# Optimization experiments

Hardware: AMD Instinct MI355X
Metric: run time of the kernel (lower is better)

## Reference

```python
import jax, jax.numpy as jnp
import numpy as np

N_ATOM, N_BOND, N_MOL, D = 250000, 250000, 10000, 64
BN_EPS = 1e-5


def _bn(x, gamma, beta):
    # torch BatchNorm1d training-mode math (biased variance)
    m = jnp.mean(x, axis=0)
    v = jnp.var(x, axis=0)
    return (x - m) * jax.lax.rsqrt(v + BN_EPS) * gamma + beta


def setup_inputs() -> dict:
    key = jax.random.key(0)
    ks = jax.random.split(key, 12)
    h = jax.random.normal(ks[0], (N_ATOM, D), jnp.float32)
    e = jax.random.normal(ks[1], (N_BOND, D), jnp.float32)
    u = jax.random.normal(ks[2], (N_MOL, D), jnp.float32)
    norm_atom = jax.random.uniform(ks[3], (N_ATOM, 1), jnp.float32)
    norm_bond = jax.random.uniform(ks[4], (N_BOND, 1), jnp.float32)
    bond_u = jax.random.randint(ks[5], (N_BOND,), 0, N_ATOM, jnp.int32)
    bond_v = jax.random.randint(ks[6], (N_BOND,), 0, N_ATOM, jnp.int32)
    atom2mol = jax.random.randint(ks[7], (N_ATOM,), 0, N_MOL, jnp.int32)
    bond2mol = jax.random.randint(ks[8], (N_BOND,), 0, N_MOL, jnp.int32)
    # 9 Linear layers A..I stacked: order A,B,C,D,E,F,G,H,I
    Ws = jax.random.normal(ks[9], (9, D, D), jnp.float32) * 0.05
    bs = jax.random.normal(ks[10], (9, D), jnp.float32) * 0.05
    bn_gamma = jnp.ones((3, D), jnp.float32)   # [e, h, u]
    bn_beta = jnp.zeros((3, D), jnp.float32)
    return dict(h=h, e=e, u=u, norm_atom=norm_atom, norm_bond=norm_bond,
                Ws=Ws, bs=bs, bn_gamma=bn_gamma, bn_beta=bn_beta,
                bond_u=bond_u, bond_v=bond_v, atom2mol=atom2mol, bond2mol=bond2mol)


def reference(h, e, u, norm_atom, norm_bond, Ws, bs, bn_gamma, bn_beta,
              bond_u, bond_v, atom2mol, bond2mol):
    lin = lambda x, i: x @ Ws[i] + bs[i]
    Ah, Dh, Eh = lin(h, 0), lin(h, 3), lin(h, 4)
    Be = lin(e, 1)
    Cu, Fu = lin(u, 2), lin(u, 5)

    # bond update: a2b (sum of Ah of both endpoints) + b2b self-loop + g2b broadcast
    e_new = Ah[bond_u] + Ah[bond_v] + Be + Cu[bond2mol]
    e_new = e_new * norm_bond                  # graph_norm
    e_new = _bn(e_new, bn_gamma[0], bn_beta[0])
    e_new = jax.nn.elu(e_new)

    # atom update: a2a self-loop + gated b2a (select_not_equal == other endpoint's Eh) + g2a
    sig = jax.nn.sigmoid(e_new)                # [N_BOND, D]
    dst = jnp.concatenate([bond_u, bond_v])    # each bond sends to both endpoints
    Eh_other = jnp.concatenate([Eh[bond_v], Eh[bond_u]])
    sig2 = jnp.concatenate([sig, sig])
    num = jax.ops.segment_sum(sig2 * Eh_other, dst, num_segments=N_ATOM)
    den = jax.ops.segment_sum(sig2, dst, num_segments=N_ATOM) + 1e-6
    h_new = Dh + num / den + Fu[atom2mol]
    h_new = h_new * norm_atom                  # graph_norm
    h_new = _bn(h_new, bn_gamma[1], bn_beta[1])
    h_new = jax.nn.elu(h_new)

    # global update: mean(Gh over atoms) + mean(He over bonds) + g2g self-loop Iu
    Gh, He, Iu = lin(h_new, 6), lin(e_new, 7), lin(u, 8)
    cnt_a = jax.ops.segment_sum(jnp.ones((N_ATOM, 1), h.dtype), atom2mol, num_segments=N_MOL)
    cnt_b = jax.ops.segment_sum(jnp.ones((N_BOND, 1), e.dtype), bond2mol, num_segments=N_MOL)
    u_new = (jax.ops.segment_sum(Gh, atom2mol, num_segments=N_MOL) / jnp.maximum(cnt_a, 1.0)
             + jax.ops.segment_sum(He, bond2mol, num_segments=N_MOL) / jnp.maximum(cnt_b, 1.0)
             + Iu)
    u_new = _bn(u_new, bn_gamma[2], bn_beta[2])
    u_new = jax.nn.elu(u_new)

    return h_new, e_new, u_new
```

## Files before the change

kernel.cpp:

```cpp
#include <hip/hip_runtime.h>
#include <cmath>

#define DD 64
#define TILE 64
#define BLK 256
#define NSLOT 64

__device__ __forceinline__ float elu_f(float x) {
  return x > 0.f ? x : expm1f(x);
}
__device__ __forceinline__ float sigmoid_fast(float x) {
  return __builtin_amdgcn_rcpf(1.f + __expf(-x));
}

__device__ __forceinline__ void fma4(float4& a, float s, const float4 b) {
  a.x = fmaf(s, b.x, a.x);
  a.y = fmaf(s, b.y, a.y);
  a.z = fmaf(s, b.z, a.z);
  a.w = fmaf(s, b.w, a.w);
}
__device__ __forceinline__ void add4(float4& a, const float4 b) {
  a.x += b.x; a.y += b.y; a.z += b.z; a.w += b.w;
}
__device__ __forceinline__ void sqacc4(float4& a, const float4 b) {
  a.x = fmaf(b.x, b.x, a.x);
  a.y = fmaf(b.y, b.y, a.y);
  a.z = fmaf(b.z, b.z, a.z);
  a.w = fmaf(b.w, b.w, a.w);
}
__device__ __forceinline__ void scale4(float4& a, float s) {
  a.x *= s; a.y *= s; a.z *= s; a.w *= s;
}

__device__ __forceinline__ void matmul_tile(const float (*xs)[DD + 4], const float (*wl)[DD],
                                            int r0, int c0, float4 acc[4]) {
#pragma unroll 2
  for (int k0 = 0; k0 < DD; k0 += 4) {
    float4 x0 = *(const float4*)&xs[r0 + 0][k0];
    float4 x1 = *(const float4*)&xs[r0 + 1][k0];
    float4 x2 = *(const float4*)&xs[r0 + 2][k0];
    float4 x3 = *(const float4*)&xs[r0 + 3][k0];
    float4 w0 = *(const float4*)&wl[k0 + 0][c0];
    float4 w1 = *(const float4*)&wl[k0 + 1][c0];
    float4 w2 = *(const float4*)&wl[k0 + 2][c0];
    float4 w3 = *(const float4*)&wl[k0 + 3][c0];
    fma4(acc[0], x0.x, w0); fma4(acc[0], x0.y, w1); fma4(acc[0], x0.z, w2); fma4(acc[0], x0.w, w3);
    fma4(acc[1], x1.x, w0); fma4(acc[1], x1.y, w1); fma4(acc[1], x1.z, w2); fma4(acc[1], x1.w, w3);
    fma4(acc[2], x2.x, w0); fma4(acc[2], x2.y, w1); fma4(acc[2], x2.z, w2); fma4(acc[2], x2.w, w3);
    fma4(acc[3], x3.x, w0); fma4(acc[3], x3.y, w1); fma4(acc[3], x3.z, w2); fma4(acc[3], x3.w, w3);
  }
}

__global__ void cnt_kernel(const int* __restrict__ a2m, int na,
                           const int* __restrict__ b2m, int nb,
                           const int* __restrict__ bu, const int* __restrict__ bv,
                           int* __restrict__ cnta_i, int* __restrict__ cntb_i,
                           int* __restrict__ deg) {
  int i = blockIdx.x * blockDim.x + threadIdx.x;
  if (i < na) {
    atomicAdd(&cnta_i[a2m[i]], 1);
  } else if (i < na + nb) {
    int b = i - na;
    atomicAdd(&cntb_i[b2m[b]], 1);
    atomicAdd(&deg[bu[b]], 1);
    atomicAdd(&deg[bv[b]], 1);
  }
}

__global__ void seg_alloc_kernel(const int* __restrict__ deg, int n,
                                 int* __restrict__ start, int* __restrict__ gcount) {
  int i = blockIdx.x * blockDim.x + threadIdx.x;
  int lane = threadIdx.x & 63;
  int d = (i < n) ? deg[i] : 0;
  int pre = d;
#pragma unroll
  for (int off = 1; off < 64; off <<= 1) {
    int t = __shfl_up(pre, off, 64);
    if (lane >= off) pre += t;
  }
  int total = __shfl(pre, 63, 64);
  int excl = pre - d;
  int base = 0;
  if (lane == 63) base = atomicAdd(gcount, total);
  base = __shfl(base, 63, 64);
  if (i < n) start[i] = base + excl;
}

__global__ void fill_kernel(const int* __restrict__ bu, const int* __restrict__ bv, int nb,
                            const int* __restrict__ start, int* __restrict__ cur,
                            int2* __restrict__ adj) {
  int b = blockIdx.x * blockDim.x + threadIdx.x;
  if (b < nb) {
    int a0 = bu[b], a1 = bv[b];
    int p = start[a0] + atomicAdd(&cur[a0], 1);
    adj[p] = make_int2(b, a1);
    int q = start[a1] + atomicAdd(&cur[a1], 1);
    adj[q] = make_int2(b, a0);
  }
}

__global__ void fill_mol_kernel(const int* __restrict__ a2m, int na,
                                const int* __restrict__ b2m, int nb,
                                const int* __restrict__ start_ma, int* __restrict__ cur_ma,
                                int* __restrict__ lista,
                                const int* __restrict__ start_mb, int* __restrict__ cur_mb,
                                int* __restrict__ listb) {
  int i = blockIdx.x * blockDim.x + threadIdx.x;
  if (i < na) {
    int m = a2m[i];
    lista[start_ma[m] + atomicAdd(&cur_ma[m], 1)] = i;
  } else if (i < na + nb) {
    int b = i - na;
    int m = b2m[b];
    listb[start_mb[m] + atomicAdd(&cur_mb[m], 1)] = b;
  }
}

__global__ __launch_bounds__(BLK) void lin2_kernel(
    const float* __restrict__ x, int nrows,
    const float* __restrict__ W0, const float* __restrict__ b0, float* __restrict__ out0,
    const float* __restrict__ W1, const float* __restrict__ b1, float* __restrict__ out1) {
  __shared__ __align__(16) float xs[TILE][DD + 4];
  __shared__ __align__(16) float w0[DD][DD];
  __shared__ __align__(16) float w1[DD][DD];
  const int tid = threadIdx.x;
  const int base = blockIdx.x * TILE;
  int rows = nrows - base; if (rows > TILE) rows = TILE;
  for (int l = tid; l < DD * DD; l += BLK) {
    int r = l >> 6, c = l & 63;
    xs[r][c] = (r < rows) ? x[(size_t)(base + r) * DD + c] : 0.f;
    w0[r][c] = W0[l];
    w1[r][c] = W1[l];
  }
  __syncthreads();
  const int tr = tid >> 4, tc = tid & 15;
  const int r0 = tr * 4, c0 = tc * 4;
  float4 accA[4], accB[4];
#pragma unroll
  for (int i = 0; i < 4; ++i) {
    accA[i] = make_float4(0.f, 0.f, 0.f, 0.f);
    accB[i] = make_float4(0.f, 0.f, 0.f, 0.f);
  }
#pragma unroll 1
  for (int k0 = 0; k0 < DD; k0 += 4) {
    float4 x0 = *(const float4*)&xs[r0 + 0][k0];
    float4 x1 = *(const float4*)&xs[r0 + 1][k0];
    float4 x2 = *(const float4*)&xs[r0 + 2][k0];
    float4 x3 = *(const float4*)&xs[r0 + 3][k0];
    float4 wa0 = *(const float4*)&w0[k0 + 0][c0];
    float4 wa1 = *(const float4*)&w0[k0 + 1][c0];
    float4 wa2 = *(const float4*)&w0[k0 + 2][c0];
    float4 wa3 = *(const float4*)&w0[k0 + 3][c0];
    float4 wb0 = *(const float4*)&w1[k0 + 0][c0];
    float4 wb1 = *(const float4*)&w1[k0 + 1][c0];
    float4 wb2 = *(const float4*)&w1[k0 + 2][c0];
    float4 wb3 = *(const float4*)&w1[k0 + 3][c0];
    fma4(accA[0], x0.x, wa0); fma4(accA[0], x0.y, wa1); fma4(accA[0], x0.z, wa2); fma4(accA[0], x0.w, wa3);
    fma4(accA[1], x1.x, wa0); fma4(accA[1], x1.y, wa1); fma4(accA[1], x1.z, wa2); fma4(accA[1], x1.w, wa3);
    fma4(accA[2], x2.x, wa0); fma4(accA[2], x2.y, wa1); fma4(accA[2], x2.z, wa2); fma4(accA[2], x2.w, wa3);
    fma4(accA[3], x3.x, wa0); fma4(accA[3], x3.y, wa1); fma4(accA[3], x3.z, wa2); fma4(accA[3], x3.w, wa3);
    fma4(accB[0], x0.x, wb0); fma4(accB[0], x0.y, wb1); fma4(accB[0], x0.z, wb2); fma4(accB[0], x0.w, wb3);
    fma4(accB[1], x1.x, wb0); fma4(accB[1], x1.y, wb1); fma4(accB[1], x1.z, wb2); fma4(accB[1], x1.w, wb3);
    fma4(accB[2], x2.x, wb0); fma4(accB[2], x2.y, wb1); fma4(accB[2], x2.z, wb2); fma4(accB[2], x2.w, wb3);
    fma4(accB[3], x3.x, wb0); fma4(accB[3], x3.y, wb1); fma4(accB[3], x3.z, wb2); fma4(accB[3], x3.w, wb3);
  }
  float4 bv0 = *(const float4*)&b0[c0];
  float4 bv1 = *(const float4*)&b1[c0];
#pragma unroll
  for (int i = 0; i < 4; ++i) {
    if (r0 + i < rows) {
      size_t rb = (size_t)(base + r0 + i) * DD + c0;
      float4 o0 = accA[i]; add4(o0, bv0);
      float4 o1 = accB[i]; add4(o1, bv1);
      *(float4*)&out0[rb] = o0;
      *(float4*)&out1[rb] = o1;
    }
  }
}

__global__ __launch_bounds__(BLK) void lin1_kernel(
    const float* __restrict__ x, int nrows,
    const float* __restrict__ W, const float* __restrict__ b, float* __restrict__ out) {
  __shared__ __align__(16) float xs[TILE][DD + 4];
  __shared__ __align__(16) float wl[DD][DD];
  const int tid = threadIdx.x;
  const int base = blockIdx.x * TILE;
  int rows = nrows - base; if (rows > TILE) rows = TILE;
  for (int l = tid; l < DD * DD; l += BLK) {
    int r = l >> 6, c = l & 63;
    xs[r][c] = (r < rows) ? x[(size_t)(base + r) * DD + c] : 0.f;
    wl[r][c] = W[l];
  }
  __syncthreads();
  const int tr = tid >> 4, tc = tid & 15;
  const int r0 = tr * 4, c0 = tc * 4;
  float4 acc[4];
#pragma unroll
  for (int i = 0; i < 4; ++i) acc[i] = make_float4(0.f, 0.f, 0.f, 0.f);
  matmul_tile(xs, wl, r0, c0, acc);
  float4 bv = *(const float4*)&b[c0];
#pragma unroll
  for (int i = 0; i < 4; ++i) {
    if (r0 + i < rows) {
      size_t rb = (size_t)(base + r0 + i) * DD + c0;
      float4 o = acc[i]; add4(o, bv);
      *(float4*)&out[rb] = o;
    }
  }
}

__global__ __launch_bounds__(BLK) void bond1_kernel(
    const float* __restrict__ e, int nrows, int ntiles,
    const float* __restrict__ W1, const float* __restrict__ b1,
    const float* __restrict__ Ah, const float* __restrict__ Cu,
    const int* __restrict__ bu, const int* __restrict__ bv, const int* __restrict__ b2m,
    const float* __restrict__ nrm,
    float* __restrict__ e_pre,
    float* __restrict__ ssum, float* __restrict__ ssq) {
  __shared__ __align__(16) float xs[TILE][DD + 4];
  __shared__ __align__(16) float wl[DD][DD];
  __shared__ int sbu[TILE], sbv[TILE], sbm[TILE];
  __shared__ float snb[TILE];
  __shared__ __align__(16) float red[16][DD];
  const int tid = threadIdx.x;
  const int tr = tid >> 4, tc = tid & 15, r0 = tr * 4, c0 = tc * 4;
  for (int l = tid; l < DD * DD; l += BLK) wl[l >> 6][l & 63] = W1[l];
  float4 bp = *(const float4*)&b1[c0];
  float4 lsum = make_float4(0.f, 0.f, 0.f, 0.f);
  float4 lsq  = make_float4(0.f, 0.f, 0.f, 0.f);
  for (int tile = blockIdx.x; tile < ntiles; tile += gridDim.x) {
    const int base = tile * TILE;
    int rows = nrows - base; if (rows > TILE) rows = TILE;
    __syncthreads();
    for (int l = tid; l < TILE * DD; l += BLK) {
      int r = l >> 6, c = l & 63;
      xs[r][c] = (r < rows) ? e[(size_t)(base + r) * DD + c] : 0.f;
    }
    if (tid < TILE) {
      bool v = tid < rows;
      int rb = base + tid;
      sbu[tid] = v ? bu[rb] : 0;
      sbv[tid] = v ? bv[rb] : 0;
      sbm[tid] = v ? b2m[rb] : 0;
      snb[tid] = v ? nrm[rb] : 0.f;
    }
    __syncthreads();
    float4 acc[4];
#pragma unroll
    for (int i = 0; i < 4; ++i) acc[i] = make_float4(0.f, 0.f, 0.f, 0.f);
    matmul_tile(xs, wl, r0, c0, acc);
#pragma unroll
    for (int i = 0; i < 4; ++i) {
      int r = r0 + i;
      if (r < rows) {
        int rb = base + r;
        float nb = snb[r];
        float4 ga = *(const float4*)&Ah[(size_t)sbu[r] * DD + c0];
        float4 gb = *(const float4*)&Ah[(size_t)sbv[r] * DD + c0];
        float4 gc = *(const float4*)&Cu[(size_t)sbm[r] * DD + c0];
        float4 o = acc[i];
        add4(o, bp); add4(o, ga); add4(o, gb); add4(o, gc);
        scale4(o, nb);
        add4(lsum, o); sqacc4(lsq, o);
        *(float4*)&e_pre[(size_t)rb * DD + c0] = o;
      }
    }
  }
  __syncthreads();
  *(float4*)&red[tr][c0] = lsum;
  __syncthreads();
  if (tid < DD) {
    float s = 0.f;
#pragma unroll
    for (int t = 0; t < 16; ++t) s += red[t][tid];
    atomicAdd(&ssum[tid], s);
  }
  __syncthreads();
  *(float4*)&red[tr][c0] = lsq;
  __syncthreads();
  if (tid < DD) {
    float s = 0.f;
#pragma unroll
    for (int t = 0; t < 16; ++t) s += red[t][tid];
    atomicAdd(&ssq[tid], s);
  }
}

__global__ void bnfinal_kernel(const float* __restrict__ ssum, const float* __restrict__ ssq,
                               const float* __restrict__ gamma, const float* __restrict__ beta,
                               float invN, float* __restrict__ scale, float* __restrict__ shift) {
  int j = threadIdx.x;
  float m = ssum[j] * invN;
  float v = ssq[j] * invN - m * m;
  float sc = gamma[j] * rsqrtf(v + 1e-5f);
  scale[j] = sc;
  shift[j] = beta[j] - m * sc;
}

__global__ void bnfinal_slots_kernel(const float* __restrict__ psum, const float* __restrict__ psq,
                                     const float* __restrict__ gamma, const float* __restrict__ beta,
                                     float invN, float* __restrict__ scale, float* __restrict__ shift) {
  int j = threadIdx.x;
  float s = 0.f, q = 0.f;
#pragma unroll 8
  for (int t = 0; t < NSLOT; ++t) {
    s += psum[t * DD + j];
    q += psq[t * DD + j];
  }
  float m = s * invN;
  float v = q * invN - m * m;
  float sc = gamma[j] * rsqrtf(v + 1e-5f);
  scale[j] = sc;
  shift[j] = beta[j] - m * sc;
}

__global__ void bn_elu_vec_kernel(float* __restrict__ x, long n4,
                                  const float* __restrict__ scale,
                                  const float* __restrict__ shift) {
  long stride = (long)gridDim.x * blockDim.x;
  for (long i = blockIdx.x * (long)blockDim.x + threadIdx.x; i < n4; i += stride) {
    float4 v = ((float4*)x)[i];
    int c0 = (int)((i & 15) << 2);
    float4 sc = *(const float4*)&scale[c0];
    float4 sh = *(const float4*)&shift[c0];
    v.x = elu_f(fmaf(v.x, sc.x, sh.x));
    v.y = elu_f(fmaf(v.y, sc.y, sh.y));
    v.z = elu_f(fmaf(v.z, sc.z, sh.z));
    v.w = elu_f(fmaf(v.w, sc.w, sh.w));
    ((float4*)x)[i] = v;
  }
}

__global__ __launch_bounds__(BLK) void agg_fused_kernel(
    const float* __restrict__ e_act, const float* __restrict__ Eh,
    const float* __restrict__ Dhb, const float* __restrict__ Fu,
    const int* __restrict__ a2m, const float* __restrict__ nrm,
    const int* __restrict__ start, const int* __restrict__ deg,
    const int2* __restrict__ adj, int na,
    float* __restrict__ hpre,
    float* __restrict__ psum, float* __restrict__ psq) {
  const int tid = threadIdx.x;
  const int lane = tid & 63;
  const int wv = tid >> 6;
  const int wid = blockIdx.x * (BLK >> 6) + wv;
  float lsum = 0.f, lsq = 0.f;
  if (wid < na) {
    float dh = Dhb[(size_t)wid * DD + lane];
    float fu = Fu[(size_t)a2m[wid] * DD + lane];
    float nr = nrm[wid];
    int s = start[wid], d = deg[wid];
    float num = 0.f, den = 0.f;
    for (int k = 0; k < d; ++k) {
      int2 ent = adj[s + k];
      float ev = e_act[(size_t)ent.x * DD + lane];
      float eh = Eh[(size_t)ent.y * DD + lane];
      float sg = sigmoid_fast(ev);
      num = fmaf(sg, eh, num);
      den += sg;
    }
    float o = (dh + num / (den + 1e-6f) + fu) * nr;
    hpre[(size_t)wid * DD + lane] = o;
    lsum = o;
    lsq = o * o;
  }
  __shared__ __align__(16) float red[BLK / 64][DD];
  red[wv][lane] = lsum;
  __syncthreads();
  if (tid < DD) {
    float s4 = red[0][tid] + red[1][tid] + red[2][tid] + red[3][tid];
    atomicAdd(&psum[(blockIdx.x & (NSLOT - 1)) * DD + tid], s4);
  }
  __syncthreads();
  red[wv][lane] = lsq;
  __syncthreads();
  if (tid < DD) {
    float s4 = red[0][tid] + red[1][tid] + red[2][tid] + red[3][tid];
    atomicAdd(&psq[(blockIdx.x & (NSLOT - 1)) * DD + tid], s4);
  }
}

__global__ __launch_bounds__(BLK) void molsum_kernel(
    const float* __restrict__ src, const int* __restrict__ start,
    const int* __restrict__ cnt, const int* __restrict__ list, int nm,
    float* __restrict__ out) {
  int wid = (int)((blockIdx.x * (unsigned)blockDim.x + threadIdx.x) >> 6);
  int lane = threadIdx.x & 63;
  if (wid >= nm) return;
  int s = start[wid], c = cnt[wid];
  float acc = 0.f;
  int k = 0;
  for (; k + 2 <= c; k += 2) {
    int i0 = list[s + k], i1 = list[s + k + 1];
    float v0 = src[(size_t)i0 * DD + lane];
    float v1 = src[(size_t)i1 * DD + lane];
    acc += v0 + v1;
  }
  if (k < c) acc += src[(size_t)list[s + k] * DD + lane];
  out[(size_t)wid * DD + lane] = acc;
}

__global__ __launch_bounds__(BLK) void global1_kernel(
    const float* __restrict__ u, int nrows,
    const float* __restrict__ W6, const float* __restrict__ W7, const float* __restrict__ W8,
    const float* __restrict__ b6, const float* __restrict__ b7, const float* __restrict__ b8,
    const float* __restrict__ msa, const float* __restrict__ msb,
    const int* __restrict__ cnta, const int* __restrict__ cntb,
    float* __restrict__ upre,
    float* __restrict__ ssum, float* __restrict__ ssq) {
  __shared__ __align__(16) float xsu[TILE][DD + 4];
  __shared__ __align__(16) float xsa[TILE][DD + 4];
  __shared__ __align__(16) float xsb[TILE][DD + 4];
  __shared__ __align__(16) float w6s[DD][DD];
  __shared__ __align__(16) float w7s[DD][DD];
  __shared__ __align__(16) float w8s[DD][DD];
  __shared__ float sfa[TILE], sfb[TILE];
  __shared__ __align__(16) float red[16][DD];
  const int tid = threadIdx.x;
  const int base = blockIdx.x * TILE;
  int rows = nrows - base; if (rows > TILE) rows = TILE;
  for (int l = tid; l < DD * DD; l += BLK) {
    int r = l >> 6, c = l & 63;
    w6s[r][c] = W6[l];
    w7s[r][c] = W7[l];
    w8s[r][c] = W8[l];
  }
  for (int l = tid; l < TILE * DD; l += BLK) {
    int r = l >> 6, c = l & 63;
    bool v = r < rows;
    float ca = 1.f, cb = 1.f;
    if (v) {
      int ia = cnta[base + r], ib = cntb[base + r];
      ca = ia > 0 ? (float)ia : 1.f;
      cb = ib > 0 ? (float)ib : 1.f;
    }
    xsu[r][c] = v ? u[(size_t)(base + r) * DD + c] : 0.f;
    xsa[r][c] = v ? msa[(size_t)(base + r) * DD + c] / ca : 0.f;
    xsb[r][c] = v ? msb[(size_t)(base + r) * DD + c] / cb : 0.f;
  }
  if (tid < TILE) {
    bool v = tid < rows;
    sfa[tid] = (v && cnta[base + tid] > 0) ? 1.f : 0.f;
    sfb[tid] = (v && cntb[base + tid] > 0) ? 1.f : 0.f;
  }
  __syncthreads();
  const int tr = tid >> 4, tc = tid & 15, r0 = tr * 4, c0 = tc * 4;
  float4 acc[4];
#pragma unroll
  for (int i = 0; i < 4; ++i) acc[i] = make_float4(0.f, 0.f, 0.f, 0.f);
  matmul_tile(xsu, w8s, r0, c0, acc);
  matmul_tile(xsa, w6s, r0, c0, acc);
  matmul_tile(xsb, w7s, r0, c0, acc);
  float4 b6v = *(const float4*)&b6[c0];
  float4 b7v = *(const float4*)&b7[c0];
  float4 b8v = *(const float4*)&b8[c0];
  float4 lsum = make_float4(0.f, 0.f, 0.f, 0.f);
  float4 lsq  = make_float4(0.f, 0.f, 0.f, 0.f);
#pragma unroll
  for (int i = 0; i < 4; ++i) {
    int r = r0 + i;
    if (r < rows) {
      size_t rb = (size_t)(base + r) * DD + c0;
      float fa = sfa[r], fb = sfb[r];
      float4 o = acc[i];
      o.x += b8v.x + fa * b6v.x + fb * b7v.x;
      o.y += b8v.y + fa * b6v.y + fb * b7v.y;
      o.z += b8v.z + fa * b6v.z + fb * b7v.z;
      o.w += b8v.w + fa * b6v.w + fb * b7v.w;
      add4(lsum, o); sqacc4(lsq, o);
      *(float4*)&upre[rb] = o;
    }
  }
  __syncthreads();
  *(float4*)&red[tr][c0] = lsum;
  __syncthreads();
  if (tid < DD) {
    float s = 0.f;
#pragma unroll
    for (int t = 0; t < 16; ++t) s += red[t][tid];
    atomicAdd(&ssum[tid], s);
  }
  __syncthreads();
  *(float4*)&red[tr][c0] = lsq;
  __syncthreads();
  if (tid < DD) {
    float s = 0.f;
#pragma unroll
    for (int t = 0; t < 16; ++t) s += red[t][tid];
    atomicAdd(&ssq[tid], s);
  }
}

extern "C" void kernel_launch(void* const* d_in, const int* in_sizes, int n_in,
                              void* d_out, int out_size, void* d_ws, size_t ws_size,
                              hipStream_t stream) {
  const float* h         = (const float*)d_in[0];
  const float* e         = (const float*)d_in[1];
  const float* u         = (const float*)d_in[2];
  const float* norm_atom = (const float*)d_in[3];
  const float* norm_bond = (const float*)d_in[4];
  const float* Ws        = (const float*)d_in[5];
  const float* bsarr     = (const float*)d_in[6];
  const float* bn_gamma  = (const float*)d_in[7];
  const float* bn_beta   = (const float*)d_in[8];
  const int* bond_u      = (const int*)d_in[9];
  const int* bond_v      = (const int*)d_in[10];
  const int* a2m         = (const int*)d_in[11];
  const int* b2m         = (const int*)d_in[12];

  const int NA = in_sizes[0] / DD;
  const int NB = in_sizes[1] / DD;
  const int NM = in_sizes[2] / DD;

  float* out_h = (float*)d_out;
  float* out_e = out_h + (size_t)NA * DD;
  float* out_u = out_e + (size_t)NB * DD;

  float* f     = (float*)d_ws;
  float* Ah    = f;
  float* Dhb   = Ah;
  float* Eh    = Ah + (size_t)NA * DD;
  float* Cu    = Eh + (size_t)NA * DD;
  float* Fu    = Cu + (size_t)NM * DD;
  float* msa   = Fu + (size_t)NM * DD;
  float* msb   = msa + (size_t)NM * DD;
  float* stats = msb + (size_t)NM * DD;
  float* sum_e = stats, *sq_e = stats + 64;
  float* sum_u = stats + 128, *sq_u = stats + 192;
  float* psum_h = stats + 256;
  float* psq_h  = psum_h + NSLOT * DD;
  int* deg     = (int*)(psq_h + NSLOT * DD);
  int* cur     = deg + NA;
  int* cnta_i  = cur + NA;
  int* cntb_i  = cnta_i + NM;
  int* cur_ma  = cntb_i + NM;
  int* cur_mb  = cur_ma + NM;
  int* gcounts = cur_mb + NM;
  float* bnp   = (float*)(gcounts + 4);
  float* sc_e = bnp, *sh_e = bnp + 64;
  float* sc_h = bnp + 128, *sh_h = bnp + 192;
  float* sc_u = bnp + 256, *sh_u = bnp + 320;
  int* start    = (int*)(bnp + 384);
  int* start_ma = start + NA;
  int* start_mb = start_ma + NM;
  int* lista    = start_mb + NM;
  int* listb    = lista + NA;
  int2* adj     = (int2*)(listb + NB);

  const float* W0 = Ws + 0 * 4096; const float* b0 = bsarr + 0 * 64;
  const float* W1 = Ws + 1 * 4096; const float* b1 = bsarr + 1 * 64;
  const float* W2 = Ws + 2 * 4096; const float* b2 = bsarr + 2 * 64;
  const float* W3 = Ws + 3 * 4096; const float* b3 = bsarr + 3 * 64;
  const float* W4 = Ws + 4 * 4096; const float* b4 = bsarr + 4 * 64;
  const float* W5 = Ws + 5 * 4096; const float* b5 = bsarr + 5 * 64;
  const float* W6 = Ws + 6 * 4096; const float* b6 = bsarr + 6 * 64;
  const float* W7 = Ws + 7 * 4096; const float* b7 = bsarr + 7 * 64;
  const float* W8 = Ws + 8 * 4096; const float* b8 = bsarr + 8 * 64;

  const int tiles_a = (NA + TILE - 1) / TILE;
  const int tiles_b = (NB + TILE - 1) / TILE;
  const int tiles_m = (NM + TILE - 1) / TILE;

  size_t zbytes = (256 + (size_t)NSLOT * DD * 2) * sizeof(float)
                + ((size_t)NA * 2 + (size_t)NM * 4 + 4) * sizeof(int);
  hipMemsetAsync(stats, 0, zbytes, stream);

  cnt_kernel<<<(NA + NB + BLK - 1) / BLK, BLK, 0, stream>>>(a2m, NA, b2m, NB,
                                                            bond_u, bond_v,
                                                            cnta_i, cntb_i, deg);
  seg_alloc_kernel<<<(NA + BLK - 1) / BLK, BLK, 0, stream>>>(deg, NA, start, gcounts + 0);
  seg_alloc_kernel<<<(NM + BLK - 1) / BLK, BLK, 0, stream>>>(cnta_i, NM, start_ma, gcounts + 1);
  seg_alloc_kernel<<<(NM + BLK - 1) / BLK, BLK, 0, stream>>>(cntb_i, NM, start_mb, gcounts + 2);
  fill_kernel<<<(NB + BLK - 1) / BLK, BLK, 0, stream>>>(bond_u, bond_v, NB, start, cur, adj);
  fill_mol_kernel<<<(NA + NB + BLK - 1) / BLK, BLK, 0, stream>>>(a2m, NA, b2m, NB,
                                                                 start_ma, cur_ma, lista,
                                                                 start_mb, cur_mb, listb);

  lin2_kernel<<<tiles_a, BLK, 0, stream>>>(h, NA, W0, b0, Ah, W4, b4, Eh);
  lin2_kernel<<<tiles_m, BLK, 0, stream>>>(u, NM, W2, b2, Cu, W5, b5, Fu);

  int nblk_b = tiles_b < 2048 ? tiles_b : 2048;
  bond1_kernel<<<nblk_b, BLK, 0, stream>>>(e, NB, tiles_b, W1, b1, Ah, Cu,
                                           bond_u, bond_v, b2m, norm_bond,
                                           out_e, sum_e, sq_e);
  bnfinal_kernel<<<1, 64, 0, stream>>>(sum_e, sq_e, bn_gamma + 0, bn_beta + 0,
                                       1.f / (float)NB, sc_e, sh_e);

  {
    long n4 = (long)NB * (DD / 4);
    int blocks = (int)((n4 + BLK - 1) / BLK); if (blocks > 2048) blocks = 2048;
    bn_elu_vec_kernel<<<blocks, BLK, 0, stream>>>(out_e, n4, sc_e, sh_e);
  }

  lin1_kernel<<<tiles_a, BLK, 0, stream>>>(h, NA, W3, b3, Dhb);

  agg_fused_kernel<<<(NA + 3) / 4, BLK, 0, stream>>>(out_e, Eh, Dhb, Fu, a2m, norm_atom,
                                                     start, deg, adj, NA,
                                                     out_h, psum_h, psq_h);
  bnfinal_slots_kernel<<<1, 64, 0, stream>>>(psum_h, psq_h, bn_gamma + 64, bn_beta + 64,
                                             1.f / (float)NA, sc_h, sh_h);

  {
    long n4 = (long)NA * (DD / 4);
    int blocks = (int)((n4 + BLK - 1) / BLK); if (blocks > 2048) blocks = 2048;
    bn_elu_vec_kernel<<<blocks, BLK, 0, stream>>>(out_h, n4, sc_h, sh_h);
  }

  molsum_kernel<<<(NM + 3) / 4, BLK, 0, stream>>>(out_h, start_ma, cnta_i, lista, NM, msa);
  molsum_kernel<<<(NM + 3) / 4, BLK, 0, stream>>>(out_e, start_mb, cntb_i, listb, NM, msb);

  global1_kernel<<<tiles_m, BLK, 0, stream>>>(u, NM, W6, W7, W8, b6, b7, b8,
                                              msa, msb, cnta_i, cntb_i,
                                              out_u, sum_u, sq_u);
  bnfinal_kernel<<<1, 64, 0, stream>>>(sum_u, sq_u, bn_gamma + 128, bn_beta + 128,
                                       1.f / (float)NM, sc_u, sh_u);
  {
    long n4 = (long)NM * (DD / 4);
    int blocks = (int)((n4 + BLK - 1) / BLK); if (blocks > 2048) blocks = 2048;
    bn_elu_vec_kernel<<<blocks, BLK, 0, stream>>>(out_u, n4, sc_u, sh_u);
  }
}
```

Before: 706.4 us.

## Spread bond BN stats over atomic slots, unroll gather loop, merge molsum launches

The bond kernel now accumulates BatchNorm partial sums into 64 slot buffers instead of a single 64-float array, which spreads the atomic contention, and the final reduction uses the slot-aware finalizer. The atom aggregation loop is unrolled by two so two gathers are in flight at once. The two molecule-sum launches are merged into one kernel that covers both atoms and bonds. Together these should cut atomic serialization, gather latency and one launch, at the cost of a larger memset and a few more registers.

```diff
diff --git a/kernel.cpp b/kernel.cpp
--- a/kernel.cpp
+++ b/kernel.cpp
@@ -216,7 +216,7 @@
     const int* __restrict__ bu, const int* __restrict__ bv, const int* __restrict__ b2m,
     const float* __restrict__ nrm,
     float* __restrict__ e_pre,
-    float* __restrict__ ssum, float* __restrict__ ssq) {
+    float* __restrict__ psum, float* __restrict__ psq) {
   __shared__ __align__(16) float xs[TILE][DD + 4];
   __shared__ __align__(16) float wl[DD][DD];
   __shared__ int sbu[TILE], sbv[TILE], sbm[TILE];
@@ -269,11 +269,12 @@
   __syncthreads();
   *(float4*)&red[tr][c0] = lsum;
   __syncthreads();
+  const int slot = (blockIdx.x & (NSLOT - 1)) * DD;
   if (tid < DD) {
     float s = 0.f;
 #pragma unroll
     for (int t = 0; t < 16; ++t) s += red[t][tid];
-    atomicAdd(&ssum[tid], s);
+    atomicAdd(&psum[slot + tid], s);
   }
   __syncthreads();
   *(float4*)&red[tr][c0] = lsq;
@@ -282,7 +283,7 @@
     float s = 0.f;
 #pragma unroll
     for (int t = 0; t < 16; ++t) s += red[t][tid];
-    atomicAdd(&ssq[tid], s);
+    atomicAdd(&psq[slot + tid], s);
   }
 }
 
@@ -350,13 +351,25 @@
     float nr = nrm[wid];
     int s = start[wid], d = deg[wid];
     float num = 0.f, den = 0.f;
-    for (int k = 0; k < d; ++k) {
-      int2 ent = adj[s + k];
-      float ev = e_act[(size_t)ent.x * DD + lane];
-      float eh = Eh[(size_t)ent.y * DD + lane];
+    int k = 0;
+    for (; k + 2 <= d; k += 2) {
+      int2 e0 = adj[s + k];
+      int2 e1 = adj[s + k + 1];
+      float ev0 = e_act[(size_t)e0.x * DD + lane];
+      float eh0 = Eh[(size_t)e0.y * DD + lane];
+      float ev1 = e_act[(size_t)e1.x * DD + lane];
+      float eh1 = Eh[(size_t)e1.y * DD + lane];
+      float sg0 = sigmoid_fast(ev0);
+      float sg1 = sigmoid_fast(ev1);
+      num = fmaf(sg0, eh0, num); den += sg0;
+      num = fmaf(sg1, eh1, num); den += sg1;
+    }
+    if (k < d) {
+      int2 e0 = adj[s + k];
+      float ev = e_act[(size_t)e0.x * DD + lane];
+      float eh = Eh[(size_t)e0.y * DD + lane];
       float sg = sigmoid_fast(ev);
-      num = fmaf(sg, eh, num);
-      den += sg;
+      num = fmaf(sg, eh, num); den += sg;
     }
     float o = (dh + num / (den + 1e-6f) + fu) * nr;
     hpre[(size_t)wid * DD + lane] = o;
@@ -379,14 +392,26 @@
   }
 }
 
-__global__ __launch_bounds__(BLK) void molsum_kernel(
-    const float* __restrict__ src, const int* __restrict__ start,
-    const int* __restrict__ cnt, const int* __restrict__ list, int nm,
-    float* __restrict__ out) {
+__global__ __launch_bounds__(BLK) void molsum2_kernel(
+    const float* __restrict__ srcA, const int* __restrict__ start_ma,
+    const int* __restrict__ cnta, const int* __restrict__ lista,
+    const float* __restrict__ srcB, const int* __restrict__ start_mb,
+    const int* __restrict__ cntb, const int* __restrict__ listb,
+    int nm, float* __restrict__ msa, float* __restrict__ msb) {
   int wid = (int)((blockIdx.x * (unsigned)blockDim.x + threadIdx.x) >> 6);
   int lane = threadIdx.x & 63;
-  if (wid >= nm) return;
-  int s = start[wid], c = cnt[wid];
+  if (wid >= 2 * nm) return;
+  const float* src;
+  const int* list;
+  float* out;
+  int m, s, c;
+  if (wid < nm) {
+    m = wid; src = srcA; list = lista; out = msa;
+    s = start_ma[m]; c = cnta[m];
+  } else {
+    m = wid - nm; src = srcB; list = listb; out = msb;
+    s = start_mb[m]; c = cntb[m];
+  }
   float acc = 0.f;
   int k = 0;
   for (; k + 2 <= c; k += 2) {
@@ -396,7 +421,7 @@
     acc += v0 + v1;
   }
   if (k < c) acc += src[(size_t)list[s + k] * DD + lane];
-  out[(size_t)wid * DD + lane] = acc;
+  out[(size_t)m * DD + lane] = acc;
 }
 
 __global__ __launch_bounds__(BLK) void global1_kernel(
@@ -524,11 +549,12 @@
   float* msa   = Fu + (size_t)NM * DD;
   float* msb   = msa + (size_t)NM * DD;
   float* stats = msb + (size_t)NM * DD;
-  float* sum_e = stats, *sq_e = stats + 64;
-  float* sum_u = stats + 128, *sq_u = stats + 192;
+  float* sum_u = stats, *sq_u = stats + 64;
   float* psum_h = stats + 256;
   float* psq_h  = psum_h + NSLOT * DD;
-  int* deg     = (int*)(psq_h + NSLOT * DD);
+  float* psum_e = psq_h + NSLOT * DD;
+  float* psq_e  = psum_e + NSLOT * DD;
+  int* deg     = (int*)(psq_e + NSLOT * DD);
   int* cur     = deg + NA;
   int* cnta_i  = cur + NA;
   int* cntb_i  = cnta_i + NM;
@@ -560,7 +586,7 @@
   const int tiles_b = (NB + TILE - 1) / TILE;
   const int tiles_m = (NM + TILE - 1) / TILE;
 
-  size_t zbytes = (256 + (size_t)NSLOT * DD * 2) * sizeof(float)
+  size_t zbytes = (256 + (size_t)NSLOT * DD * 4) * sizeof(float)
                 + ((size_t)NA * 2 + (size_t)NM * 4 + 4) * sizeof(int);
   hipMemsetAsync(stats, 0, zbytes, stream);
 
@@ -581,9 +607,9 @@
   int nblk_b = tiles_b < 2048 ? tiles_b : 2048;
   bond1_kernel<<<nblk_b, BLK, 0, stream>>>(e, NB, tiles_b, W1, b1, Ah, Cu,
                                            bond_u, bond_v, b2m, norm_bond,
-                                           out_e, sum_e, sq_e);
-  bnfinal_kernel<<<1, 64, 0, stream>>>(sum_e, sq_e, bn_gamma + 0, bn_beta + 0,
-                                       1.f / (float)NB, sc_e, sh_e);
+                                           out_e, psum_e, psq_e);
+  bnfinal_slots_kernel<<<1, 64, 0, stream>>>(psum_e, psq_e, bn_gamma + 0, bn_beta + 0,
+                                             1.f / (float)NB, sc_e, sh_e);
 
   {
     long n4 = (long)NB * (DD / 4);
@@ -605,8 +631,9 @@
     bn_elu_vec_kernel<<<blocks, BLK, 0, stream>>>(out_h, n4, sc_h, sh_h);
   }
 
-  molsum_kernel<<<(NM + 3) / 4, BLK, 0, stream>>>(out_h, start_ma, cnta_i, lista, NM, msa);
-  molsum_kernel<<<(NM + 3) / 4, BLK, 0, stream>>>(out_e, start_mb, cntb_i, listb, NM, msb);
+  molsum2_kernel<<<(2 * NM + 3) / 4, BLK, 0, stream>>>(out_h, start_ma, cnta_i, lista,
+                                                       out_e, start_mb, cntb_i, listb,
+                                                       NM, msa, msb);
 
   global1_kernel<<<tiles_m, BLK, 0, stream>>>(u, NM, W6, W7, W8, b6, b7, b8,
                                               msa, msb, cnta_i, cntb_i,
```

Result: faster. 654.3 us (-7.4%).
